# Optimization experiments

Hardware: AMD Instinct MI355X
Metric: run time of the kernel (lower is better)

Reference implementation:

```python
import jax, jax.numpy as jnp
import numpy as np

N_NODES = 10000
N_EDGES = 640000
NF = 128      # n_features
NH = 128      # n_hidden
NT = 128      # n_targets
LN_EPS = 1e-5


def _layer_norm(h, gamma, beta):
    mu = jnp.mean(h, axis=-1, keepdims=True)
    var = jnp.var(h, axis=-1, keepdims=True)
    return (h - mu) * jax.lax.rsqrt(var + LN_EPS) * gamma + beta


def _mlp(h, W1, b1, gamma, beta, W2, b2):
    h = jax.nn.relu(h @ W1 + b1)
    h = _layer_norm(h, gamma, beta)
    return h @ W2 + b2


def setup_inputs() -> dict:
    key = jax.random.key(0)
    ks = jax.random.split(key, 12)
    s_in = 1.0 / np.sqrt(NF + NH)
    s_h = 1.0 / np.sqrt(NH)
    return {
        "x": jax.random.normal(ks[0], (N_NODES, NF), dtype=jnp.float32),
        "edge_idx": jax.random.randint(ks[1], (2, N_EDGES), 0, N_NODES, dtype=jnp.int32),
        "edge_attr": jax.random.normal(ks[2], (N_EDGES, NH), dtype=jnp.float32),
        # node_mlp_1 params
        "W1a": jax.random.normal(ks[3], (NF + NH, NH), dtype=jnp.float32) * s_in,
        "b1a": jnp.zeros((NH,), dtype=jnp.float32),
        "g1": jnp.ones((NH,), dtype=jnp.float32),
        "be1": jnp.zeros((NH,), dtype=jnp.float32),
        "W1b": jax.random.normal(ks[4], (NH, NH), dtype=jnp.float32) * s_h,
        "b1b": jnp.zeros((NH,), dtype=jnp.float32),
        # node_mlp_2 params
        "W2a": jax.random.normal(ks[5], (NF + NH, NH), dtype=jnp.float32) * s_in,
        "b2a": jnp.zeros((NH,), dtype=jnp.float32),
        "g2": jnp.ones((NH,), dtype=jnp.float32),
        "be2": jnp.zeros((NH,), dtype=jnp.float32),
        "W2b": jax.random.normal(ks[6], (NH, NT), dtype=jnp.float32) * s_h,
        "b2b": jnp.zeros((NT,), dtype=jnp.float32),
    }


def reference(x, edge_idx, edge_attr, W1a, b1a, g1, be1, W1b, b1b,
              W2a, b2a, g2, be2, W2b, b2b):
    row, col = edge_idx[0], edge_idx[1]
    # gather source-node features and run per-edge MLP
    h = jnp.concatenate([x[col], edge_attr], axis=1)        # [E, NF+NH]
    h = _mlp(h, W1a, b1a, g1, be1, W1b, b1b)                 # [E, NH]
    # scatter_mean into target nodes
    sums = jax.ops.segment_sum(h, row, num_segments=N_NODES)
    cnt = jax.ops.segment_sum(jnp.ones((h.shape[0],), h.dtype), row,
                              num_segments=N_NODES)
    agg = sums / jnp.maximum(cnt, 1.0)[:, None]              # [N, NH]
    out = jnp.concatenate([x, agg], axis=1)                  # [N, NF+NH]
    return _mlp(out, W2a, b2a, g2, be2, W2b, b2b)            # [N, NT]
```

## Files before the change

kernel.cpp:

```cpp
#include <hip/hip_runtime.h>
#include <hip/hip_bf16.h>

#define NN 10000
#define NE 640000
#define NF 128
#define NH 128
#define NT 128
#define KA 256
#define LN_EPS 1e-5f

typedef __bf16 bf16x8 __attribute__((ext_vector_type(8)));
typedef float floatx4 __attribute__((ext_vector_type(4)));
typedef float nfloat4 __attribute__((ext_vector_type(4)));

__device__ inline unsigned short f2bf(float f) {
    unsigned int u = __float_as_uint(f);
    u += 0x7FFFu + ((u >> 16) & 1u);
    return (unsigned short)(u >> 16);
}

__device__ inline bf16x8 load_frag(const unsigned short* p) {
    uint4 u = *(const uint4*)p;
    return __builtin_bit_cast(bf16x8, u);
}

__device__ inline bf16x8 cvt8(nfloat4 v0, nfloat4 v1) {
    bf16x8 r;
    r[0] = (__bf16)v0.x; r[1] = (__bf16)v0.y; r[2] = (__bf16)v0.z; r[3] = (__bf16)v0.w;
    r[4] = (__bf16)v1.x; r[5] = (__bf16)v1.y; r[6] = (__bf16)v1.z; r[7] = (__bf16)v1.w;
    return r;
}

__global__ __launch_bounds__(256) void conv_weights(
    const float* __restrict__ W1a, const float* __restrict__ W1b,
    const float* __restrict__ W2a, const float* __restrict__ W2b,
    unsigned short* __restrict__ wp1a, unsigned short* __restrict__ wp1b,
    unsigned short* __restrict__ wp2a, unsigned short* __restrict__ wp2b)
{
    int tid = blockIdx.x * 256 + threadIdx.x;
    const float* src;
    unsigned short* dst;
    int t, nks;
    if (tid < 4096)        { src = W1a; dst = wp1a; t = tid;         nks = 8; }
    else if (tid < 6144)   { src = W1b; dst = wp1b; t = tid - 4096;  nks = 4; }
    else if (tid < 10240)  { src = W2a; dst = wp2a; t = tid - 6144;  nks = 8; }
    else if (tid < 12288)  { src = W2b; dst = wp2b; t = tid - 10240; nks = 4; }
    else return;

    const int f = t >> 6, l = t & 63;
    const int ct = f / nks, ks = f - ct * nks;
    const int n  = ct * 16 + (l & 15);
    const int k0 = ks * 32 + (l >> 4) * 8;
    unsigned short tmp[8];
#pragma unroll
    for (int j = 0; j < 8; ++j)
        tmp[j] = f2bf(src[(k0 + j) * 128 + n]);
    *(uint4*)&dst[t * 8] = *(const uint4*)tmp;
}

__global__ __launch_bounds__(256) void hist_kernel(
    const int* __restrict__ row, int* __restrict__ hist)
{
    int e = blockIdx.x * 256 + threadIdx.x;
    if (e < NE) atomicAdd(&hist[row[e]], 1);
}

__global__ __launch_bounds__(256) void scan_kernel(
    const int* __restrict__ hist, int* __restrict__ row_start,
    int* __restrict__ cursor)
{
    __shared__ int partials[256];
    const int t = threadIdx.x;
    const int base = t * 40;
    int s = 0;
    for (int i = 0; i < 40; ++i) {
        int b = base + i;
        if (b < NN) s += hist[b];
    }
    partials[t] = s;
    __syncthreads();
    int pre = 0;
    for (int i = 0; i < t; ++i) pre += partials[i];
    int run = pre;
    for (int i = 0; i < 40; ++i) {
        int b = base + i;
        if (b < NN) {
            row_start[b] = run;
            cursor[b] = run;
            run += hist[b];
        }
    }
    if (t == 255) row_start[NN] = NE;
}

__global__ __launch_bounds__(256) void scatter_kernel(
    const int* __restrict__ row, int* __restrict__ cursor,
    int* __restrict__ perm)
{
    int e = blockIdx.x * 256 + threadIdx.x;
    if (e < NE) {
        int p = atomicAdd(&cursor[row[e]], 1);
        perm[p] = e;
    }
}

__global__ __launch_bounds__(256, 4) void edge_mlp_kernel(
    const float* __restrict__ x,
    const int* __restrict__ erow, const int* __restrict__ ecol,
    const float* __restrict__ eattr,
    const int* __restrict__ perm,
    const unsigned short* __restrict__ wp1a, const float* __restrict__ b1a,
    const float* __restrict__ g1, const float* __restrict__ be1,
    const unsigned short* __restrict__ wp1b,
    float* __restrict__ sums)
{
    __shared__ __align__(16) float accbuf[64 * 128];
    __shared__ int rows_s[64];

    const int wave = threadIdx.x >> 6;
    const int lane = threadIdx.x & 63;
    const int lm   = lane & 15;
    const int lq4  = lane >> 4;
    const int e0   = blockIdx.x * 64;

    if (threadIdx.x < 64)
        rows_s[threadIdx.x] = erow[perm[e0 + threadIdx.x]];

    const int e    = perm[e0 + wave * 16 + lm];
    const int scol = ecol[e];
    const nfloat4* xr = (const nfloat4*)(x + (size_t)scol * NF) + lq4 * 2;
    const nfloat4* ar = (const nfloat4*)(eattr + (size_t)e * NH) + lq4 * 2;

    bf16x8 a1[8];
#pragma unroll
    for (int ks = 0; ks < 4; ++ks) {
        nfloat4 v0 = xr[ks * 8];
        nfloat4 v1 = xr[ks * 8 + 1];
        a1[ks] = cvt8(v0, v1);
    }
#pragma unroll
    for (int ks = 0; ks < 4; ++ks) {
        nfloat4 v0 = __builtin_nontemporal_load(ar + ks * 8);
        nfloat4 v1 = __builtin_nontemporal_load(ar + ks * 8 + 1);
        a1[4 + ks] = cvt8(v0, v1);
    }

    floatx4 acc1[8];
#pragma unroll
    for (int ct = 0; ct < 8; ++ct) {
        floatx4 acc = {0.f, 0.f, 0.f, 0.f};
        const unsigned short* wr = wp1a + (ct * 8 * 64 + lane) * 8;
#pragma unroll
        for (int ks = 0; ks < 8; ++ks) {
            bf16x8 b = load_frag(wr + ks * 512);
            acc = __builtin_amdgcn_mfma_f32_16x16x32_bf16(a1[ks], b, acc, 0, 0, 0);
        }
        acc1[ct] = acc;
    }

    float sum_[4] = {0, 0, 0, 0}, sq_[4] = {0, 0, 0, 0};
#pragma unroll
    for (int ct = 0; ct < 8; ++ct) {
        const float bb = b1a[ct * 16 + lm];
#pragma unroll
        for (int i = 0; i < 4; ++i) {
            float v = acc1[ct][i] + bb;
            v = fmaxf(v, 0.f);
            acc1[ct][i] = v;
            sum_[i] += v;
            sq_[i]  += v * v;
        }
    }
#pragma unroll
    for (int m = 1; m < 16; m <<= 1) {
#pragma unroll
        for (int i = 0; i < 4; ++i) {
            sum_[i] += __shfl_xor(sum_[i], m, 64);
            sq_[i]  += __shfl_xor(sq_[i],  m, 64);
        }
    }
    float mu[4], rs[4];
#pragma unroll
    for (int i = 0; i < 4; ++i) {
        mu[i] = sum_[i] * (1.f / NH);
        float var = sq_[i] * (1.f / NH) - mu[i] * mu[i];
        rs[i] = rsqrtf(var + LN_EPS);
    }

    unsigned short* Tw = (unsigned short*)(accbuf + wave * 16 * 128);
#pragma unroll
    for (int ct = 0; ct < 8; ++ct) {
        const int c = ct * 16 + lm;
        const float gg = g1[c], bb = be1[c];
#pragma unroll
        for (int i = 0; i < 4; ++i) {
            float nv = (acc1[ct][i] - mu[i]) * rs[i] * gg + bb;
            Tw[(lq4 * 4 + i) * 136 + c] = __builtin_bit_cast(unsigned short, (__bf16)nv);
        }
    }
    asm volatile("" ::: "memory");

    bf16x8 a2[4];
#pragma unroll
    for (int ks = 0; ks < 4; ++ks)
        a2[ks] = load_frag(&Tw[lm * 136 + ks * 32 + lq4 * 8]);

#pragma unroll
    for (int ct = 0; ct < 8; ++ct) {
        floatx4 acc = {0.f, 0.f, 0.f, 0.f};
        const unsigned short* wr = wp1b + (ct * 4 * 64 + lane) * 8;
#pragma unroll
        for (int ks = 0; ks < 4; ++ks) {
            bf16x8 b = load_frag(wr + ks * 512);
            acc = __builtin_amdgcn_mfma_f32_16x16x32_bf16(a2[ks], b, acc, 0, 0, 0);
        }
        const int c = ct * 16 + lm;
#pragma unroll
        for (int i = 0; i < 4; ++i) {
            const int r = wave * 16 + lq4 * 4 + i;
            accbuf[r * 128 + ((c + r * 4) & 127)] = acc[i];
        }
    }
    __syncthreads();

    {
        const int t = threadIdx.x;
        const int cc = t & 127;
        const int jb = (t >> 7) * 32;
        float a = 0.f;
        int cur = rows_s[jb];
#pragma unroll 4
        for (int j = jb; j < jb + 32; ++j) {
            a += accbuf[j * 128 + ((cc + j * 4) & 127)];
            int nxt = (j + 1 < jb + 32) ? rows_s[j + 1] : -1;
            if (nxt != cur) {
                atomicAdd(&sums[cur * NH + cc], a);
                a = 0.f;
                cur = nxt;
            }
        }
    }
}

__global__ __launch_bounds__(256) void node_mlp_kernel(
    const float* __restrict__ x,
    const float* __restrict__ sums, const int* __restrict__ row_start,
    const float* __restrict__ b1b,
    const unsigned short* __restrict__ wp2a, const float* __restrict__ b2a,
    const float* __restrict__ g2, const float* __restrict__ be2,
    const unsigned short* __restrict__ wp2b, const float* __restrict__ b2b,
    float* __restrict__ out)
{
    __shared__ unsigned short Atile[4][16][KA + 8];
    __shared__ unsigned short Ttile[4][16][NH + 8];

    const int wave = threadIdx.x >> 6;
    const int lane = threadIdx.x & 63;
    const int n0 = blockIdx.x * 64 + wave * 16;

    {
        const int lrow = lane >> 2;
        const int lq   = lane & 3;
        int n = n0 + lrow;
        if (n >= NN) n = NN - 1;
        const int cntn = row_start[n + 1] - row_start[n];
        const float inv  = (cntn > 0) ? (1.f / (float)cntn) : 1.f;
        const float addb = (cntn > 0) ? 1.f : 0.f;
        const float4* xr = (const float4*)(x + n * NF);
        const float4* sr = (const float4*)(sums + n * NH);
        const float4* br = (const float4*)b1b;
        unsigned short* Ar = &Atile[wave][lrow][0];
#pragma unroll
        for (int it = 0; it < 8; ++it) {
            int c4 = lq + it * 4;
            float4 v = xr[c4];
            uint2 w;
            w.x = (unsigned)f2bf(v.x) | ((unsigned)f2bf(v.y) << 16);
            w.y = (unsigned)f2bf(v.z) | ((unsigned)f2bf(v.w) << 16);
            *(uint2*)&Ar[c4 * 4] = w;
            float4 v2 = sr[c4];
            float4 bv = br[c4];
            float a0 = v2.x * inv + addb * bv.x;
            float a1 = v2.y * inv + addb * bv.y;
            float a2 = v2.z * inv + addb * bv.z;
            float a3 = v2.w * inv + addb * bv.w;
            uint2 w2;
            w2.x = (unsigned)f2bf(a0) | ((unsigned)f2bf(a1) << 16);
            w2.y = (unsigned)f2bf(a2) | ((unsigned)f2bf(a3) << 16);
            *(uint2*)&Ar[128 + c4 * 4] = w2;
        }
    }
    __syncthreads();

    const int lm  = lane & 15;
    const int lq4 = lane >> 4;

    bf16x8 a1[8];
#pragma unroll
    for (int ks = 0; ks < 8; ++ks)
        a1[ks] = load_frag(&Atile[wave][lm][ks * 32 + lq4 * 8]);

    floatx4 acc1[8];
#pragma unroll
    for (int ct = 0; ct < 8; ++ct) {
        floatx4 acc = {0.f, 0.f, 0.f, 0.f};
        const unsigned short* wr = wp2a + (ct * 8 * 64 + lane) * 8;
#pragma unroll
        for (int ks = 0; ks < 8; ++ks) {
            bf16x8 b = load_frag(wr + ks * 512);
            acc = __builtin_amdgcn_mfma_f32_16x16x32_bf16(a1[ks], b, acc, 0, 0, 0);
        }
        acc1[ct] = acc;
    }

    float sum_[4] = {0, 0, 0, 0}, sq_[4] = {0, 0, 0, 0};
#pragma unroll
    for (int ct = 0; ct < 8; ++ct) {
        const float bb = b2a[ct * 16 + lm];
#pragma unroll
        for (int i = 0; i < 4; ++i) {
            float v = acc1[ct][i] + bb;
            v = fmaxf(v, 0.f);
            acc1[ct][i] = v;
            sum_[i] += v;
            sq_[i]  += v * v;
        }
    }
#pragma unroll
    for (int m = 1; m < 16; m <<= 1) {
#pragma unroll
        for (int i = 0; i < 4; ++i) {
            sum_[i] += __shfl_xor(sum_[i], m, 64);
            sq_[i]  += __shfl_xor(sq_[i],  m, 64);
        }
    }
    float mu[4], rs[4];
#pragma unroll
    for (int i = 0; i < 4; ++i) {
        mu[i] = sum_[i] * (1.f / NH);
        float var = sq_[i] * (1.f / NH) - mu[i] * mu[i];
        rs[i] = rsqrtf(var + LN_EPS);
    }
#pragma unroll
    for (int ct = 0; ct < 8; ++ct) {
        const int c = ct * 16 + lm;
        const float gg = g2[c], bb = be2[c];
#pragma unroll
        for (int i = 0; i < 4; ++i) {
            float nv = (acc1[ct][i] - mu[i]) * rs[i] * gg + bb;
            Ttile[wave][lq4 * 4 + i][c] = f2bf(nv);
        }
    }
    __syncthreads();

    bf16x8 a2[4];
#pragma unroll
    for (int ks = 0; ks < 4; ++ks)
        a2[ks] = load_frag(&Ttile[wave][lm][ks * 32 + lq4 * 8]);

#pragma unroll
    for (int ct = 0; ct < 8; ++ct) {
        floatx4 acc = {0.f, 0.f, 0.f, 0.f};
        const unsigned short* wr = wp2b + (ct * 4 * 64 + lane) * 8;
#pragma unroll
        for (int ks = 0; ks < 4; ++ks) {
            bf16x8 b = load_frag(wr + ks * 512);
            acc = __builtin_amdgcn_mfma_f32_16x16x32_bf16(a2[ks], b, acc, 0, 0, 0);
        }
        const int c = ct * 16 + lm;
        const float bb = b2b[c];
#pragma unroll
        for (int i = 0; i < 4; ++i) {
            int n = n0 + lq4 * 4 + i;
            if (n < NN) out[n * NT + c] = acc[i] + bb;
        }
    }
}

extern "C" void kernel_launch(void* const* d_in, const int* in_sizes, int n_in,
                              void* d_out, int out_size, void* d_ws, size_t ws_size,
                              hipStream_t stream) {
    const float* x     = (const float*)d_in[0];
    const int*   eidx  = (const int*)d_in[1];
    const float* eattr = (const float*)d_in[2];
    const float* W1a = (const float*)d_in[3];
    const float* b1a = (const float*)d_in[4];
    const float* g1  = (const float*)d_in[5];
    const float* be1 = (const float*)d_in[6];
    const float* W1b = (const float*)d_in[7];
    const float* b1b = (const float*)d_in[8];
    const float* W2a = (const float*)d_in[9];
    const float* b2a = (const float*)d_in[10];
    const float* g2  = (const float*)d_in[11];
    const float* be2 = (const float*)d_in[12];
    const float* W2b = (const float*)d_in[13];
    const float* b2b = (const float*)d_in[14];

    char* ws = (char*)d_ws;
    float* sums     = (float*)ws;
    int*   hist     = (int*)(ws + 5120000);
    int*   cursor   = (int*)(ws + 5160000);
    int*   row_start= (int*)(ws + 5200000);
    int*   perm     = (int*)(ws + 5240064);
    unsigned short* wp1a = (unsigned short*)(ws + 7800064);
    unsigned short* wp1b = (unsigned short*)(ws + 7865600);
    unsigned short* wp2a = (unsigned short*)(ws + 7898368);
    unsigned short* wp2b = (unsigned short*)(ws + 7963904);

    const int* erow = eidx;
    const int* ecol = eidx + NE;

    (void)hipMemsetAsync(ws, 0, 5160000, stream);
    conv_weights<<<48, 256, 0, stream>>>(W1a, W1b, W2a, W2b, wp1a, wp1b, wp2a, wp2b);
    hist_kernel<<<(NE + 255) / 256, 256, 0, stream>>>(erow, hist);
    scan_kernel<<<1, 256, 0, stream>>>(hist, row_start, cursor);
    scatter_kernel<<<(NE + 255) / 256, 256, 0, stream>>>(erow, cursor, perm);
    edge_mlp_kernel<<<NE / 64, 256, 0, stream>>>(x, erow, ecol, eattr, perm,
                                                 wp1a, b1a, g1, be1, wp1b, sums);
    node_mlp_kernel<<<(NN + 63) / 64, 256, 0, stream>>>(x, sums, row_start, b1b,
                                                        wp2a, b2a, g2, be2, wp2b, b2b,
                                                        (float*)d_out);
}
```

Before: 773.9 us.

## Stage edge inputs through LDS for coalesced loads and prefetch first weight tiles

Each group of four lanes now reads contiguous 128-byte chunks of x and edge_attr rows, converts them to bf16 and writes them into an LDS tile, then reads MFMA A-fragments back from LDS. The old scheme had each lane fetch strided pieces of a row, which is less coalesced. The first weight-tile fragments of both GEMMs are issued early so their latency overlaps the gather. The output buffer swaps XOR-style swizzling for a padded stride of 132. The cost is extra LDS traffic, a larger LDS footprint and more registers held by the prefetched fragments.

```diff
diff --git a/kernel.cpp b/kernel.cpp
--- a/kernel.cpp
+++ b/kernel.cpp
@@ -29,6 +29,10 @@
     r[0] = (__bf16)v0.x; r[1] = (__bf16)v0.y; r[2] = (__bf16)v0.z; r[3] = (__bf16)v0.w;
     r[4] = (__bf16)v1.x; r[5] = (__bf16)v1.y; r[6] = (__bf16)v1.z; r[7] = (__bf16)v1.w;
     return r;
+}
+
+__device__ inline void lds_fence() {
+    asm volatile("s_waitcnt lgkmcnt(0)" ::: "memory");
 }
 
 __global__ __launch_bounds__(256) void conv_weights(
@@ -114,7 +118,7 @@
     const unsigned short* __restrict__ wp1b,
     float* __restrict__ sums)
 {
-    __shared__ __align__(16) float accbuf[64 * 128];
+    __shared__ __align__(16) float smem[64 * 132];
     __shared__ int rows_s[64];
 
     const int wave = threadIdx.x >> 6;
@@ -126,24 +130,42 @@
     if (threadIdx.x < 64)
         rows_s[threadIdx.x] = erow[perm[e0 + threadIdx.x]];
 
-    const int e    = perm[e0 + wave * 16 + lm];
-    const int scol = ecol[e];
-    const nfloat4* xr = (const nfloat4*)(x + (size_t)scol * NF) + lq4 * 2;
-    const nfloat4* ar = (const nfloat4*)(eattr + (size_t)e * NH) + lq4 * 2;
-
+    bf16x8 bpre[8];
+#pragma unroll
+    for (int ks = 0; ks < 8; ++ks)
+        bpre[ks] = load_frag(&wp1a[(ks * 64 + lane) * 8]);
+
+    unsigned short* At = (unsigned short*)smem;
+    {
+        const int lrow = lane >> 2;
+        const int lq   = lane & 3;
+        const int e = perm[e0 + wave * 16 + lrow];
+        const int scol = ecol[e];
+        const nfloat4* xr = (const nfloat4*)(x + (size_t)scol * NF);
+        const nfloat4* ar = (const nfloat4*)(eattr + (size_t)e * NH);
+        unsigned short* Ar = At + (wave * 16 + lrow) * 264;
+#pragma unroll
+        for (int it = 0; it < 4; ++it) {
+            const int g = lq + it * 4;
+            nfloat4 v0 = xr[g * 2];
+            nfloat4 v1 = xr[g * 2 + 1];
+            *(uint4*)&Ar[g * 8] = __builtin_bit_cast(uint4, cvt8(v0, v1));
+        }
+#pragma unroll
+        for (int it = 0; it < 4; ++it) {
+            const int g = lq + it * 4;
+            nfloat4 v0 = __builtin_nontemporal_load(ar + g * 2);
+            nfloat4 v1 = __builtin_nontemporal_load(ar + g * 2 + 1);
+            *(uint4*)&Ar[128 + g * 8] = __builtin_bit_cast(uint4, cvt8(v0, v1));
+        }
+    }
+    lds_fence();
+
+    unsigned short* Tw = At + wave * 16 * 264;
     bf16x8 a1[8];
 #pragma unroll
-    for (int ks = 0; ks < 4; ++ks) {
-        nfloat4 v0 = xr[ks * 8];
-        nfloat4 v1 = xr[ks * 8 + 1];
-        a1[ks] = cvt8(v0, v1);
-    }
-#pragma unroll
-    for (int ks = 0; ks < 4; ++ks) {
-        nfloat4 v0 = __builtin_nontemporal_load(ar + ks * 8);
-        nfloat4 v1 = __builtin_nontemporal_load(ar + ks * 8 + 1);
-        a1[4 + ks] = cvt8(v0, v1);
-    }
+    for (int ks = 0; ks < 8; ++ks)
+        a1[ks] = load_frag(&Tw[lm * 264 + ks * 32 + lq4 * 8]);
 
     floatx4 acc1[8];
 #pragma unroll
@@ -152,11 +174,16 @@
         const unsigned short* wr = wp1a + (ct * 8 * 64 + lane) * 8;
 #pragma unroll
         for (int ks = 0; ks < 8; ++ks) {
-            bf16x8 b = load_frag(wr + ks * 512);
+            bf16x8 b = (ct == 0) ? bpre[ks] : load_frag(wr + ks * 512);
             acc = __builtin_amdgcn_mfma_f32_16x16x32_bf16(a1[ks], b, acc, 0, 0, 0);
         }
         acc1[ct] = acc;
     }
+
+    bf16x8 b2pre[4];
+#pragma unroll
+    for (int ks = 0; ks < 4; ++ks)
+        b2pre[ks] = load_frag(&wp1b[(ks * 64 + lane) * 8]);
 
     float sum_[4] = {0, 0, 0, 0}, sq_[4] = {0, 0, 0, 0};
 #pragma unroll
@@ -187,7 +214,6 @@
         rs[i] = rsqrtf(var + LN_EPS);
     }
 
-    unsigned short* Tw = (unsigned short*)(accbuf + wave * 16 * 128);
 #pragma unroll
     for (int ct = 0; ct < 8; ++ct) {
         const int c = ct * 16 + lm;
@@ -195,15 +221,15 @@
 #pragma unroll
         for (int i = 0; i < 4; ++i) {
             float nv = (acc1[ct][i] - mu[i]) * rs[i] * gg + bb;
-            Tw[(lq4 * 4 + i) * 136 + c] = __builtin_bit_cast(unsigned short, (__bf16)nv);
-        }
-    }
-    asm volatile("" ::: "memory");
+            Tw[(lq4 * 4 + i) * 264 + c] = __builtin_bit_cast(unsigned short, (__bf16)nv);
+        }
+    }
+    lds_fence();
 
     bf16x8 a2[4];
 #pragma unroll
     for (int ks = 0; ks < 4; ++ks)
-        a2[ks] = load_frag(&Tw[lm * 136 + ks * 32 + lq4 * 8]);
+        a2[ks] = load_frag(&Tw[lm * 264 + ks * 32 + lq4 * 8]);
 
 #pragma unroll
     for (int ct = 0; ct < 8; ++ct) {
@@ -211,14 +237,14 @@
         const unsigned short* wr = wp1b + (ct * 4 * 64 + lane) * 8;
 #pragma unroll
         for (int ks = 0; ks < 4; ++ks) {
-            bf16x8 b = load_frag(wr + ks * 512);
+            bf16x8 b = (ct == 0) ? b2pre[ks] : load_frag(wr + ks * 512);
             acc = __builtin_amdgcn_mfma_f32_16x16x32_bf16(a2[ks], b, acc, 0, 0, 0);
         }
         const int c = ct * 16 + lm;
 #pragma unroll
         for (int i = 0; i < 4; ++i) {
             const int r = wave * 16 + lq4 * 4 + i;
-            accbuf[r * 128 + ((c + r * 4) & 127)] = acc[i];
+            smem[r * 132 + c] = acc[i];
         }
     }
     __syncthreads();
@@ -231,7 +257,7 @@
         int cur = rows_s[jb];
 #pragma unroll 4
         for (int j = jb; j < jb + 32; ++j) {
-            a += accbuf[j * 128 + ((cc + j * 4) & 127)];
+            a += smem[j * 132 + cc];
             int nxt = (j + 1 < jb + 32) ? rows_s[j + 1] : -1;
             if (nxt != cur) {
                 atomicAdd(&sums[cur * NH + cc], a);
```

Result: faster. 733.0 us (-5.3%).
